# Performance work log

Hardware: AMD Instinct MI355X
Metric: run time of the kernel (lower is better)

Reference implementation:

```python
import jax, jax.numpy as jnp
import numpy as np

B, L, D, H = 2, 2048, 1024, 16
DH = D // H


def setup_inputs() -> dict:
    key = jax.random.key(0)
    ks = jax.random.split(key, 5)
    bound = 1.0 / D ** 0.5
    x = jax.random.normal(ks[0], (B, L, D), dtype=jnp.float32)
    # causal mask: 0 means masked out
    mask = jnp.tril(jnp.ones((L, L), dtype=jnp.int32))[None].repeat(B, axis=0)
    Wq = jax.random.uniform(ks[1], (D, D), jnp.float32, -bound, bound)
    Wk = jax.random.uniform(ks[2], (D, D), jnp.float32, -bound, bound)
    Wv = jax.random.uniform(ks[3], (D, D), jnp.float32, -bound, bound)
    Wo = jax.random.uniform(ks[4], (D, D), jnp.float32, -bound, bound)
    return {"x": x, "mask": mask, "Wq": Wq, "Wk": Wk, "Wv": Wv, "Wo": Wo}


def _split_heads(t):
    # (B, L, D) -> (B, H, L, DH)
    b, l, _ = t.shape
    return t.reshape(b, l, H, DH).transpose(0, 2, 1, 3)


def reference(x, mask, Wq, Wk, Wv, Wo):
    # projections: torch Linear does x @ W.T with W:(out,in)
    q = _split_heads(x @ Wq.T)  # (B,H,L,DH)
    k = _split_heads(x @ Wk.T)
    v = _split_heads(x @ Wv.T)
    scores = jnp.einsum('bhqd,bhkd->bhqk', q, k) / jnp.sqrt(jnp.float32(DH))
    m = mask[:, None, :, :]  # (B,1,L,L)
    scores = jnp.where(m == 0, jnp.float32(-jnp.inf), scores)
    attn = jax.nn.softmax(scores, axis=-1)
    out = jnp.einsum('bhqk,bhkd->bhqd', attn, v)  # (B,H,L,DH)
    out = out.transpose(0, 2, 1, 3).reshape(x.shape[0], x.shape[1], D)
    return out @ Wo.T
```

## Files before the change

kernel.cpp:

```cpp
#include <hip/hip_runtime.h>
#include <stdint.h>


typedef unsigned short u16;
typedef __attribute__((ext_vector_type(8))) short short8;
typedef __attribute__((ext_vector_type(4))) float f32x4;
typedef __attribute__((ext_vector_type(4))) unsigned int uint4v;

#define NEG_BIG (-1e30f)
#define QSCALE 0.18033688011112042f

__device__ __forceinline__ f32x4 mfma16(short8 a, short8 b, f32x4 c) {
    return __builtin_amdgcn_mfma_f32_16x16x32_bf16(a, b, c, 0, 0, 0);
}

__device__ __forceinline__ u16 f2bf(float f) {
    uint32_t u = __float_as_uint(f);
    u += 0x7fffu + ((u >> 16) & 1u);
    return (u16)(u >> 16);
}

#if __has_builtin(__builtin_amdgcn_cvt_pk_bf16_f32)
__device__ __forceinline__ unsigned int f2bf_pk(float a, float b) {
    return __builtin_bit_cast(unsigned int, __builtin_amdgcn_cvt_pk_bf16_f32(a, b));
}
#else
__device__ __forceinline__ unsigned int f2bf_pk(float a, float b) {
    return (unsigned int)f2bf(a) | ((unsigned int)f2bf(b) << 16);
}
#endif

__device__ __forceinline__ void load_lds_16B(const u16* g, u16* lds_base) {
    __builtin_amdgcn_global_load_lds(
        (__attribute__((address_space(1))) void*)(uintptr_t)(const void*)g,
        (__attribute__((address_space(3))) void*)lds_base,
        16, 0, 0);
}

__global__ __launch_bounds__(256) void cvt_kernel(
    const float* __restrict__ x, const float* __restrict__ wq, const float* __restrict__ wk,
    const float* __restrict__ wv, const float* __restrict__ wo, u16* __restrict__ dst)
{
    const int gid = blockIdx.x * 256 + threadIdx.x;
    const float* src; size_t off;
    if (gid < 524288)      { src = x;  off = (size_t)gid * 8; }
    else if (gid < 655360) { src = wq; off = (size_t)(gid - 524288) * 8; }
    else if (gid < 786432) { src = wk; off = (size_t)(gid - 655360) * 8; }
    else if (gid < 917504) { src = wv; off = (size_t)(gid - 786432) * 8; }
    else                   { src = wo; off = (size_t)(gid - 917504) * 8; }
    float4 a = *(const float4*)(src + off);
    float4 b = *(const float4*)(src + off + 4);
    uint4v u = { f2bf_pk(a.x, a.y), f2bf_pk(a.z, a.w),
                 f2bf_pk(b.x, b.y), f2bf_pk(b.z, b.w) };
    *(uint4v*)(dst + (size_t)gid * 8) = u;
}

__device__ __forceinline__ void gemm_bt_128x128(
    const u16* __restrict__ A, const u16* __restrict__ Bw,
    u16* at, u16* bt, int m0, int n0, f32x4 acc[4][4])
{
    const int tid  = threadIdx.x;
    const int w    = tid >> 6, lane = tid & 63;
    const int quad = lane >> 4, l15 = lane & 15;
    const int wm   = (w >> 1) * 64, wn = (w & 1) * 64;
    const int srow0 = w * 32 + (lane >> 2);
    const int sp    = lane & 3;

    for (int k0 = 0; k0 < 1024; k0 += 32) {
#pragma unroll
        for (int c = 0; c < 2; ++c) {
            int row = srow0 + c * 16;
            int g   = sp ^ ((row >> 1) & 3);
            load_lds_16B(A  + (size_t)(m0 + row) * 1024 + k0 + g * 8, at + (w * 32 + c * 16) * 32);
            load_lds_16B(Bw + (size_t)(n0 + row) * 1024 + k0 + g * 8, bt + (w * 32 + c * 16) * 32);
        }
        __syncthreads();
        short8 af[4], bf[4];
#pragma unroll
        for (int rf = 0; rf < 4; ++rf) {
            int ra = wm + rf * 16 + l15, sa = quad ^ ((ra >> 1) & 3);
            af[rf] = *(const short8*)(at + ra * 32 + sa * 8);
            int rb = wn + rf * 16 + l15, sb = quad ^ ((rb >> 1) & 3);
            bf[rf] = *(const short8*)(bt + rb * 32 + sb * 8);
        }
#pragma unroll
        for (int rf = 0; rf < 4; ++rf)
#pragma unroll
            for (int cf = 0; cf < 4; ++cf)
                acc[rf][cf] = mfma16(af[rf], bf[cf], acc[rf][cf]);
        __syncthreads();
    }
}

__global__ __launch_bounds__(256, 3) void qkv_gemm(
    const u16* __restrict__ xb, const u16* __restrict__ Wq, const u16* __restrict__ Wk,
    const u16* __restrict__ Wv, u16* __restrict__ qbuf, u16* __restrict__ kbuf,
    u16* __restrict__ vtbuf)
{
    __shared__ __align__(16) u16 at[128 * 32];
    __shared__ __align__(16) u16 bt[128 * 32];
    const int m0  = blockIdx.x * 128;
    const int by  = blockIdx.y;
    const int sel = by >> 3;
    const int n0  = (by & 7) * 128;
    const u16* Wsel = sel == 0 ? Wq : (sel == 1 ? Wk : Wv);

    f32x4 acc[4][4];
    const f32x4 z = {0.f, 0.f, 0.f, 0.f};
#pragma unroll
    for (int i = 0; i < 4; ++i)
#pragma unroll
        for (int j = 0; j < 4; ++j) acc[i][j] = z;

    gemm_bt_128x128(xb, Wsel, at, bt, m0, n0, acc);

    const int tid  = threadIdx.x, w = tid >> 6, lane = tid & 63;
    const int quad = lane >> 4, l15 = lane & 15;
    const int wm   = (w >> 1) * 64, wn = (w & 1) * 64;

    if (sel < 2) {
        u16* dst = sel == 0 ? qbuf : kbuf;
        const float scl = sel == 0 ? QSCALE : 1.0f;
#pragma unroll
        for (int rf = 0; rf < 4; ++rf)
#pragma unroll
            for (int cf = 0; cf < 4; ++cf) {
                int n = n0 + wn + cf * 16 + l15;
                int h = n >> 6, dh = n & 63;
#pragma unroll
                for (int r = 0; r < 4; ++r) {
                    int m = m0 + wm + rf * 16 + quad * 4 + r;
                    int b = m >> 11, l = m & 2047;
                    dst[(((size_t)(b * 16 + h)) * 2048 + l) * 64 + dh] = f2bf(acc[rf][cf][r] * scl);
                }
            }
    } else {
#pragma unroll
        for (int rf = 0; rf < 4; ++rf)
#pragma unroll
            for (int cf = 0; cf < 4; ++cf) {
                int n = n0 + wn + cf * 16 + l15;
                int h = n >> 6, dh = n & 63;
                int m = m0 + wm + rf * 16 + quad * 4;
                int b = m >> 11, l = m & 2047;
                ushort4 pk;
                pk.x = f2bf(acc[rf][cf][0]);
                pk.y = f2bf(acc[rf][cf][1]);
                pk.z = f2bf(acc[rf][cf][2]);
                pk.w = f2bf(acc[rf][cf][3]);
                *(ushort4*)(vtbuf + (((size_t)(b * 16 + h)) * 64 + dh) * 2048 + l) = pk;
            }
    }
}

__global__ __launch_bounds__(512, 4) void attn_kernel(
    const u16* __restrict__ qbuf, const u16* __restrict__ kbuf,
    const u16* __restrict__ vtbuf, u16* __restrict__ attn)
{
    __shared__ __align__(16) u16 kt[2][64 * 64];
    __shared__ __align__(16) u16 vt[2][64 * 64];
    __shared__ __align__(16) u16 pt[8 * 16 * 64];

    const int tid  = threadIdx.x, w = tid >> 6, lane = tid & 63;
    const int quad = lane >> 4, l15 = lane & 15;
    const int bh   = blockIdx.y;
    const int jq   = (blockIdx.y & 16) ? (int)blockIdx.x : (15 - (int)blockIdx.x);
    const int q0   = jq * 128;
    const int qw   = q0 + w * 16;

    const u16* qbase = qbuf  + (size_t)bh * 2048 * 64;
    const u16* kbase = kbuf  + (size_t)bh * 2048 * 64;
    const u16* vbase = vtbuf + (size_t)bh * 64 * 2048;
    u16* pw = pt + w * (16 * 64);
    const int b = bh >> 4, h = bh & 15;

    const f32x4 z = {0.f, 0.f, 0.f, 0.f};

    short8 qf[2];
#pragma unroll
    for (int ks = 0; ks < 2; ++ks)
        qf[ks] = *(const short8*)(qbase + (size_t)(qw + l15) * 64 + ks * 32 + quad * 8);

    f32x4 o[4];
    float mrun = NEG_BIG, lrun = 0.f;
#pragma unroll
    for (int df = 0; df < 4; ++df) o[df] = z;

    auto stage = [&](int t, int buf) {
        const int k0 = t * 64;
        int row = w * 8 + (lane >> 3);
        int g   = (lane & 7) ^ (row & 7);
        load_lds_16B(kbase + (size_t)(k0 + row) * 64 + g * 8, kt[buf] + (w * 8) * 64);
        load_lds_16B(vbase + (size_t)row * 2048 + k0 + g * 8, vt[buf] + (w * 8) * 64);
    };

    const int ntiles = 2 * jq + 2;
    stage(0, 0);
    for (int t = 0; t < ntiles; ++t) {
        __syncthreads();
        if (t + 1 < ntiles) stage(t + 1, (t + 1) & 1);
        const int k0 = t * 64;
        if (k0 <= qw + 15) {
            const u16* ktb = kt[t & 1];
            const u16* vtb = vt[t & 1];
            f32x4 st[4];
#pragma unroll
            for (int nf = 0; nf < 4; ++nf) st[nf] = z;
#pragma unroll
            for (int ks = 0; ks < 2; ++ks)
#pragma unroll
                for (int nf = 0; nf < 4; ++nf) {
                    int row = nf * 16 + l15;
                    int ph  = (ks * 4 + quad) ^ (row & 7);
                    short8 kf = *(const short8*)(ktb + row * 64 + ph * 8);
                    st[nf] = mfma16(kf, qf[ks], st[nf]);
                }
            if (k0 + 63 > qw) {
                int qrow = qw + l15;
#pragma unroll
                for (int nf = 0; nf < 4; ++nf)
#pragma unroll
                    for (int r = 0; r < 4; ++r) {
                        int key = k0 + nf * 16 + quad * 4 + r;
                        if (key > qrow) st[nf][r] = NEG_BIG;
                    }
            }
            {
                float mx = st[0][0];
#pragma unroll
                for (int nf = 0; nf < 4; ++nf)
#pragma unroll
                    for (int r = 0; r < 4; ++r) mx = fmaxf(mx, st[nf][r]);
                mx = fmaxf(mx, __shfl_xor(mx, 16));
                mx = fmaxf(mx, __shfl_xor(mx, 32));
                float mnew = fmaxf(mrun, mx);
                float alpha = exp2f(mrun - mnew);
                float sum = 0.f;
#pragma unroll
                for (int nf = 0; nf < 4; ++nf)
#pragma unroll
                    for (int r = 0; r < 4; ++r) {
                        float p = exp2f(st[nf][r] - mnew);
                        st[nf][r] = p;
                        sum += p;
                    }
                sum += __shfl_xor(sum, 16);
                sum += __shfl_xor(sum, 32);
                lrun = lrun * alpha + sum;
                mrun = mnew;
#pragma unroll
                for (int df = 0; df < 4; ++df) o[df] *= alpha;
            }
#pragma unroll
            for (int nf = 0; nf < 4; ++nf) {
                int ph = (nf * 2 + (quad >> 1)) ^ (l15 & 7);
                uint2 pk2;
                pk2.x = f2bf_pk(st[nf][0], st[nf][1]);
                pk2.y = f2bf_pk(st[nf][2], st[nf][3]);
                *(uint2*)(pw + l15 * 64 + ph * 8 + (quad & 1) * 4) = pk2;
            }
#pragma unroll
            for (int ks2 = 0; ks2 < 2; ++ks2) {
                int phb = (ks2 * 4 + quad) ^ (l15 & 7);
                short8 pb = *(const short8*)(pw + l15 * 64 + phb * 8);
#pragma unroll
                for (int df = 0; df < 4; ++df) {
                    int row = df * 16 + l15;
                    int ph  = (ks2 * 4 + quad) ^ (row & 7);
                    short8 vf = *(const short8*)(vtb + row * 64 + ph * 8);
                    o[df] = mfma16(vf, pb, o[df]);
                }
            }
        }
    }

    {
        float inv = 1.f / lrun;
        int qrow = qw + l15;
        u16* obase = attn + ((size_t)(b * 2048 + qrow)) * 1024 + h * 64;
#pragma unroll
        for (int df = 0; df < 4; ++df)
#pragma unroll
            for (int r = 0; r < 4; ++r) {
                int dh = df * 16 + quad * 4 + r;
                obase[dh] = f2bf(o[df][r] * inv);
            }
    }
}

__global__ __launch_bounds__(256, 3) void oproj_gemm(
    const u16* __restrict__ attn, const u16* __restrict__ Wo, float* __restrict__ out)
{
    __shared__ __align__(16) u16 at[128 * 32];
    __shared__ __align__(16) u16 bt[128 * 32];
    const int m0 = blockIdx.x * 128;
    const int n0 = blockIdx.y * 128;

    f32x4 acc[4][4];
    const f32x4 z = {0.f, 0.f, 0.f, 0.f};
#pragma unroll
    for (int i = 0; i < 4; ++i)
#pragma unroll
        for (int j = 0; j < 4; ++j) acc[i][j] = z;

    gemm_bt_128x128(attn, Wo, at, bt, m0, n0, acc);

    const int tid  = threadIdx.x, w = tid >> 6, lane = tid & 63;
    const int quad = lane >> 4, l15 = lane & 15;
    const int wm   = (w >> 1) * 64, wn = (w & 1) * 64;
#pragma unroll
    for (int rf = 0; rf < 4; ++rf)
#pragma unroll
        for (int cf = 0; cf < 4; ++cf) {
            int n = n0 + wn + cf * 16 + l15;
#pragma unroll
            for (int r = 0; r < 4; ++r) {
                int m = m0 + wm + rf * 16 + quad * 4 + r;
                out[(size_t)m * 1024 + n] = acc[rf][cf][r];
            }
        }
}

extern "C" void kernel_launch(void* const* d_in, const int* in_sizes, int n_in,
                              void* d_out, int out_size, void* d_ws, size_t ws_size,
                              hipStream_t stream) {
    const float* x  = (const float*)d_in[0];
    const float* Wq = (const float*)d_in[2];
    const float* Wk = (const float*)d_in[3];
    const float* Wv = (const float*)d_in[4];
    const float* Wo = (const float*)d_in[5];

    u16* ws    = (u16*)d_ws;
    const size_t M = 1024 * 1024;
    u16* qbuf  = ws;
    u16* kbuf  = ws + 4 * M;
    u16* vtb   = ws + 8 * M;
    u16* attnb = ws + 12 * M;
    u16* cvtb  = ws + 16 * M;
    u16* xb    = cvtb;
    u16* wqb   = cvtb + 4 * M;
    u16* wkb   = cvtb + 5 * M;
    u16* wvb   = cvtb + 6 * M;
    u16* wob   = cvtb + 7 * M;
    float* out = (float*)d_out;

    cvt_kernel<<<4096, 256, 0, stream>>>(x, Wq, Wk, Wv, Wo, cvtb);
    qkv_gemm<<<dim3(32, 24), 256, 0, stream>>>(xb, wqb, wkb, wvb, qbuf, kbuf, vtb);
    attn_kernel<<<dim3(16, 32), 512, 0, stream>>>(qbuf, kbuf, vtb, attnb);
    oproj_gemm<<<dim3(32, 8), 256, 0, stream>>>(attnb, wob, out);
}
```

Measured before the change: 210.5 us.

## Interleave causal query rows across warps and shrink output-projection tiles

The attention kernel now gives each block a mix of short and long causal query rows: four warps take early 16-row strips and four take late strips. The goal is to even out per-block work, at the cost of every block looping over nearly the full key range while short-row warps sit idle. The output-projection GEMM switches from 128x128 to 128x64 tiles with its own inline single-buffered K loop, doubling the grid to 512 blocks to fill more CUs. The smaller tiles reduce reuse per block and give up whatever pipelining the shared GEMM helper had.

```diff
diff --git a/kernel.cpp b/kernel.cpp
--- a/kernel.cpp
+++ b/kernel.cpp
@@ -164,9 +164,9 @@
     const int tid  = threadIdx.x, w = tid >> 6, lane = tid & 63;
     const int quad = lane >> 4, l15 = lane & 15;
     const int bh   = blockIdx.y;
-    const int jq   = (blockIdx.y & 16) ? (int)blockIdx.x : (15 - (int)blockIdx.x);
-    const int q0   = jq * 128;
-    const int qw   = q0 + w * 16;
+    const int bx   = blockIdx.x;
+    const int s    = bx + 16 * (w < 4 ? w : 11 - w);
+    const int qw   = s * 16;
 
     const u16* qbase = qbuf  + (size_t)bh * 2048 * 64;
     const u16* kbase = kbuf  + (size_t)bh * 2048 * 64;
@@ -194,7 +194,7 @@
         load_lds_16B(vbase + (size_t)row * 2048 + k0 + g * 8, vt[buf] + (w * 8) * 64);
     };
 
-    const int ntiles = 2 * jq + 2;
+    const int ntiles = ((16 * (bx + 112) + 15) >> 6) + 1;
     stage(0, 0);
     for (int t = 0; t < ntiles; ++t) {
         __syncthreads();
@@ -292,26 +292,60 @@
     const u16* __restrict__ attn, const u16* __restrict__ Wo, float* __restrict__ out)
 {
     __shared__ __align__(16) u16 at[128 * 32];
-    __shared__ __align__(16) u16 bt[128 * 32];
+    __shared__ __align__(16) u16 bt[64 * 32];
     const int m0 = blockIdx.x * 128;
-    const int n0 = blockIdx.y * 128;
-
-    f32x4 acc[4][4];
-    const f32x4 z = {0.f, 0.f, 0.f, 0.f};
-#pragma unroll
-    for (int i = 0; i < 4; ++i)
-#pragma unroll
-        for (int j = 0; j < 4; ++j) acc[i][j] = z;
-
-    gemm_bt_128x128(attn, Wo, at, bt, m0, n0, acc);
+    const int n0 = blockIdx.y * 64;
 
     const int tid  = threadIdx.x, w = tid >> 6, lane = tid & 63;
     const int quad = lane >> 4, l15 = lane & 15;
-    const int wm   = (w >> 1) * 64, wn = (w & 1) * 64;
+    const int wm   = (w >> 1) * 64, wn = (w & 1) * 32;
+    const int srow0 = w * 32 + (lane >> 2);
+    const int srowb = w * 16 + (lane >> 2);
+    const int sp    = lane & 3;
+
+    f32x4 acc[4][2];
+    const f32x4 z = {0.f, 0.f, 0.f, 0.f};
+#pragma unroll
+    for (int i = 0; i < 4; ++i)
+#pragma unroll
+        for (int j = 0; j < 2; ++j) acc[i][j] = z;
+
+    for (int k0 = 0; k0 < 1024; k0 += 32) {
+#pragma unroll
+        for (int c = 0; c < 2; ++c) {
+            int row = srow0 + c * 16;
+            int g   = sp ^ ((row >> 1) & 3);
+            load_lds_16B(attn + (size_t)(m0 + row) * 1024 + k0 + g * 8, at + (w * 32 + c * 16) * 32);
+        }
+        {
+            int row = srowb;
+            int g   = sp ^ ((row >> 1) & 3);
+            load_lds_16B(Wo + (size_t)(n0 + row) * 1024 + k0 + g * 8, bt + (w * 16) * 32);
+        }
+        __syncthreads();
+        short8 af[4], bf[2];
+#pragma unroll
+        for (int rf = 0; rf < 4; ++rf) {
+            int ra = wm + rf * 16 + l15, sa = quad ^ ((ra >> 1) & 3);
+            af[rf] = *(const short8*)(at + ra * 32 + sa * 8);
+        }
+#pragma unroll
+        for (int cf = 0; cf < 2; ++cf) {
+            int rb = wn + cf * 16 + l15, sb = quad ^ ((rb >> 1) & 3);
+            bf[cf] = *(const short8*)(bt + rb * 32 + sb * 8);
+        }
+#pragma unroll
+        for (int rf = 0; rf < 4; ++rf)
+#pragma unroll
+            for (int cf = 0; cf < 2; ++cf)
+                acc[rf][cf] = mfma16(af[rf], bf[cf], acc[rf][cf]);
+        __syncthreads();
+    }
+
 #pragma unroll
     for (int rf = 0; rf < 4; ++rf)
 #pragma unroll
-        for (int cf = 0; cf < 4; ++cf) {
+        for (int cf = 0; cf < 2; ++cf) {
             int n = n0 + wn + cf * 16 + l15;
 #pragma unroll
             for (int r = 0; r < 4; ++r) {
@@ -347,5 +381,5 @@
     cvt_kernel<<<4096, 256, 0, stream>>>(x, Wq, Wk, Wv, Wo, cvtb);
     qkv_gemm<<<dim3(32, 24), 256, 0, stream>>>(xb, wqb, wkb, wvb, qbuf, kbuf, vtb);
     attn_kernel<<<dim3(16, 32), 512, 0, stream>>>(qbuf, kbuf, vtb, attnb);
-    oproj_gemm<<<dim3(32, 8), 256, 0, stream>>>(attnb, wob, out);
-}
+    oproj_gemm<<<dim3(32, 16), 256, 0, stream>>>(attnb, wob, out);
+}
```

After: 219.5 us. 1.04x slower.
